# Performance work log

Hardware: AMD Instinct MI355X
Metric: run time of the kernel (lower is better)

The kernel has to match this reference:

```python
import jax, jax.numpy as jnp
import numpy as np

NUM_FEATURES = 50


def _build_port_feature_mask(num_node_features: int = NUM_FEATURES) -> np.ndarray:
    """(F, 6) mask: port p has track if any connect/port-revenue feature for p is nonzero."""
    mask = np.zeros((num_node_features, 6), dtype=np.float32)
    feat_idx = 23
    for i in range(6):
        for j in range(i):
            mask[feat_idx, i] = 1.0
            mask[feat_idx, j] = 1.0
            feat_idx += 1
    for i in range(6):
        for k in range(2):
            mask[38 + i * 2 + k, i] = 1.0
    return mask


def setup_inputs() -> dict:
    key = jax.random.key(0)
    k1, k2 = jax.random.split(key)
    B, N, F = 16, 1024, NUM_FEATURES
    node_features = jax.random.normal(k1, (B, N, F), dtype=jnp.float32)
    direction_matrix = jax.random.randint(k2, (N, N), 0, 7, dtype=jnp.int32)
    port_feature_mask = jnp.asarray(_build_port_feature_mask(F))
    return {
        "node_features": node_features,
        "direction_matrix": direction_matrix,
        "port_feature_mask": port_feature_mask,
    }


def reference(node_features, direction_matrix, port_feature_mask):
    B, N, _ = node_features.shape
    # (B, N, 6): per-hex, per-port track indicator
    port_activity = node_features @ port_feature_mask
    port_has_track = (port_activity > 0).astype(node_features.dtype)

    dir_mat = direction_matrix.astype(jnp.int32)
    adj_mask = (dir_mat != 6).astype(node_features.dtype)  # (N, N)
    dir_clamped = jnp.minimum(dir_mat, 5)                  # (N, N)
    opp_clamped = jnp.minimum((dir_mat + 3) % 6, 5)        # (N, N)

    i_idx = jnp.arange(N)[:, None]  # row index i, broadcasts with (N, N)
    j_idx = jnp.arange(N)[None, :]  # col index j
    # src[b, i, j] = port_has_track[b, i, dir_clamped[i, j]]
    src_ports = port_has_track[:, i_idx, dir_clamped]  # (B, N, N)
    # dst[b, i, j] = port_has_track[b, j, opp_clamped[i, j]]
    dst_ports = port_has_track[:, j_idx, opp_clamped]  # (B, N, N)

    return src_ports * dst_ports * adj_mask[None, :, :]
```

## Files before the change

### kernel.cpp

```cpp
#include <hip/hip_runtime.h>

#define N_NODES 1024
#define B_SZ 16
#define F_SZ 50

typedef float f32x4 __attribute__((ext_vector_type(4)));

__global__ __launch_bounds__(64) void ports_kernel(
        const float* __restrict__ nf,
        unsigned char* __restrict__ bits) {
    int idx = blockIdx.x * 64 + threadIdx.x;
    const float* r = nf + (size_t)idx * F_SZ;

    float f[27];
    #pragma unroll
    for (int q = 0; q < 27; ++q) f[q] = r[23 + q];

    float a0 = (((((f[0]  + f[1])  + f[3])  + f[6])  + f[10]) + f[15]) + f[16];
    float a1 = (((((f[0]  + f[2])  + f[4])  + f[7])  + f[11]) + f[17]) + f[18];
    float a2 = (((((f[1]  + f[2])  + f[5])  + f[8])  + f[12]) + f[19]) + f[20];
    float a3 = (((((f[3]  + f[4])  + f[5])  + f[9])  + f[13]) + f[21]) + f[22];
    float a4 = (((((f[6]  + f[7])  + f[8])  + f[9])  + f[14]) + f[23]) + f[24];
    float a5 = (((((f[10] + f[11]) + f[12]) + f[13]) + f[14]) + f[25]) + f[26];

    unsigned m = 0;
    m |= (a0 > 0.0f) ? 1u  : 0u;
    m |= (a1 > 0.0f) ? 2u  : 0u;
    m |= (a2 > 0.0f) ? 4u  : 0u;
    m |= (a3 > 0.0f) ? 8u  : 0u;
    m |= (a4 > 0.0f) ? 16u : 0u;
    m |= (a5 > 0.0f) ? 32u : 0u;
    bits[idx] = (unsigned char)m;
}

__global__ __launch_bounds__(256) void connect_kernel(
        const int* __restrict__ dir,
        const unsigned char* __restrict__ bits,
        float* __restrict__ out) {
    const int bi = blockIdx.x;
    const int t = threadIdx.x;
    const int b = bi >> 10;
    const int i = bi & (N_NODES - 1);

    int4 d = ((const int4*)(dir + (size_t)i * N_NODES))[t];
    uchar4 dv4 = ((const uchar4*)(bits + b * N_NODES))[t];
    unsigned tb[4] = {dv4.x, dv4.y, dv4.z, dv4.w};
    const unsigned s = bits[b * N_NODES + i];

    int dvv[4] = {d.x, d.y, d.z, d.w};
    f32x4 o;
    #pragma unroll
    for (int k = 0; k < 4; ++k) {
        int dval = dvv[k];
        unsigned am = (dval != 6) ? 1u : 0u;
        unsigned ds = (unsigned)min(dval, 5);
        unsigned os = (unsigned)min((dval + 3) % 6, 5);
        o[k] = ((s >> ds) & (tb[k] >> os) & am & 1u) ? 1.0f : 0.0f;
    }
    __builtin_nontemporal_store(
        o, (f32x4*)(out + (size_t)bi * N_NODES) + t);
}

extern "C" void kernel_launch(void* const* d_in, const int* in_sizes, int n_in,
                              void* d_out, int out_size, void* d_ws, size_t ws_size,
                              hipStream_t stream) {
    const float* nf  = (const float*)d_in[0];
    const int*   dir = (const int*)d_in[1];
    float* out = (float*)d_out;
    unsigned char* bits = (unsigned char*)d_ws;

    ports_kernel<<<(B_SZ * N_NODES) / 64, 64, 0, stream>>>(nf, bits);
    connect_kernel<<<B_SZ * N_NODES, 256, 0, stream>>>(dir, bits, out);
}
```

Baseline: 21.21 us.

## Precompute packed byte direction codes in prep kernel and read bytes in connect

```diff
diff --git a/kernel.cpp b/kernel.cpp
--- a/kernel.cpp
+++ b/kernel.cpp
@@ -6,35 +6,58 @@
 
 typedef float f32x4 __attribute__((ext_vector_type(4)));
 
-__global__ __launch_bounds__(64) void ports_kernel(
+__global__ __launch_bounds__(256) void prep_kernel(
         const float* __restrict__ nf,
-        unsigned char* __restrict__ bits) {
-    int idx = blockIdx.x * 64 + threadIdx.x;
-    const float* r = nf + (size_t)idx * F_SZ;
+        const int* __restrict__ dir,
+        unsigned char* __restrict__ bits,
+        unsigned char* __restrict__ pdir) {
+    const int q = blockIdx.x;
+    const int t = threadIdx.x;
 
-    float f[27];
-    #pragma unroll
-    for (int q = 0; q < 27; ++q) f[q] = r[23 + q];
+    if (q < 64) {
+        const int idx = q * 256 + t;
+        const float* r = nf + (size_t)idx * F_SZ;
+        float f[27];
+        #pragma unroll
+        for (int x = 0; x < 27; ++x) f[x] = r[23 + x];
 
-    float a0 = (((((f[0]  + f[1])  + f[3])  + f[6])  + f[10]) + f[15]) + f[16];
-    float a1 = (((((f[0]  + f[2])  + f[4])  + f[7])  + f[11]) + f[17]) + f[18];
-    float a2 = (((((f[1]  + f[2])  + f[5])  + f[8])  + f[12]) + f[19]) + f[20];
-    float a3 = (((((f[3]  + f[4])  + f[5])  + f[9])  + f[13]) + f[21]) + f[22];
-    float a4 = (((((f[6]  + f[7])  + f[8])  + f[9])  + f[14]) + f[23]) + f[24];
-    float a5 = (((((f[10] + f[11]) + f[12]) + f[13]) + f[14]) + f[25]) + f[26];
+        float a0 = (((((f[0]  + f[1])  + f[3])  + f[6])  + f[10]) + f[15]) + f[16];
+        float a1 = (((((f[0]  + f[2])  + f[4])  + f[7])  + f[11]) + f[17]) + f[18];
+        float a2 = (((((f[1]  + f[2])  + f[5])  + f[8])  + f[12]) + f[19]) + f[20];
+        float a3 = (((((f[3]  + f[4])  + f[5])  + f[9])  + f[13]) + f[21]) + f[22];
+        float a4 = (((((f[6]  + f[7])  + f[8])  + f[9])  + f[14]) + f[23]) + f[24];
+        float a5 = (((((f[10] + f[11]) + f[12]) + f[13]) + f[14]) + f[25]) + f[26];
 
-    unsigned m = 0;
-    m |= (a0 > 0.0f) ? 1u  : 0u;
-    m |= (a1 > 0.0f) ? 2u  : 0u;
-    m |= (a2 > 0.0f) ? 4u  : 0u;
-    m |= (a3 > 0.0f) ? 8u  : 0u;
-    m |= (a4 > 0.0f) ? 16u : 0u;
-    m |= (a5 > 0.0f) ? 32u : 0u;
-    bits[idx] = (unsigned char)m;
+        unsigned m = 0;
+        m |= (a0 > 0.0f) ? 1u  : 0u;
+        m |= (a1 > 0.0f) ? 2u  : 0u;
+        m |= (a2 > 0.0f) ? 4u  : 0u;
+        m |= (a3 > 0.0f) ? 8u  : 0u;
+        m |= (a4 > 0.0f) ? 16u : 0u;
+        m |= (a5 > 0.0f) ? 32u : 0u;
+        bits[idx] = (unsigned char)m;
+    } else {
+        const int e4 = (q - 64) * 256 + t;
+        int4 d = ((const int4*)dir)[e4];
+        int dv[4] = {d.x, d.y, d.z, d.w};
+        unsigned pk[4];
+        #pragma unroll
+        for (int k = 0; k < 4; ++k) {
+            int dval = dv[k];
+            unsigned adj = (dval != 6) ? 1u : 0u;
+            unsigned ds = (unsigned)min(dval, 5);
+            unsigned os = (unsigned)min((dval + 3) % 6, 5);
+            pk[k] = (adj << 6) | (os << 3) | ds;
+        }
+        uchar4 o;
+        o.x = (unsigned char)pk[0]; o.y = (unsigned char)pk[1];
+        o.z = (unsigned char)pk[2]; o.w = (unsigned char)pk[3];
+        ((uchar4*)pdir)[e4] = o;
+    }
 }
 
 __global__ __launch_bounds__(256) void connect_kernel(
-        const int* __restrict__ dir,
+        const unsigned char* __restrict__ pdir,
         const unsigned char* __restrict__ bits,
         float* __restrict__ out) {
     const int bi = blockIdx.x;
@@ -42,23 +65,20 @@
     const int b = bi >> 10;
     const int i = bi & (N_NODES - 1);
 
-    int4 d = ((const int4*)(dir + (size_t)i * N_NODES))[t];
-    uchar4 dv4 = ((const uchar4*)(bits + b * N_NODES))[t];
-    unsigned tb[4] = {dv4.x, dv4.y, dv4.z, dv4.w};
+    uchar4 p4 = ((const uchar4*)(pdir + (size_t)i * N_NODES))[t];
+    uchar4 t4 = ((const uchar4*)(bits + b * N_NODES))[t];
     const unsigned s = bits[b * N_NODES + i];
+    unsigned pv[4] = {p4.x, p4.y, p4.z, p4.w};
+    unsigned tv[4] = {t4.x, t4.y, t4.z, t4.w};
 
-    int dvv[4] = {d.x, d.y, d.z, d.w};
     f32x4 o;
     #pragma unroll
     for (int k = 0; k < 4; ++k) {
-        int dval = dvv[k];
-        unsigned am = (dval != 6) ? 1u : 0u;
-        unsigned ds = (unsigned)min(dval, 5);
-        unsigned os = (unsigned)min((dval + 3) % 6, 5);
-        o[k] = ((s >> ds) & (tb[k] >> os) & am & 1u) ? 1.0f : 0.0f;
+        unsigned p = pv[k];
+        o[k] = ((s >> (p & 7u)) & (tv[k] >> ((p >> 3) & 7u)) & (p >> 6) & 1u)
+                   ? 1.0f : 0.0f;
     }
-    __builtin_nontemporal_store(
-        o, (f32x4*)(out + (size_t)bi * N_NODES) + t);
+    *((f32x4*)(out + (size_t)bi * N_NODES) + t) = o;
 }
 
 extern "C" void kernel_launch(void* const* d_in, const int* in_sizes, int n_in,
@@ -68,7 +88,8 @@
     const int*   dir = (const int*)d_in[1];
     float* out = (float*)d_out;
     unsigned char* bits = (unsigned char*)d_ws;
+    unsigned char* pdir = (unsigned char*)d_ws + 16384;
 
-    ports_kernel<<<(B_SZ * N_NODES) / 64, 64, 0, stream>>>(nf, bits);
-    connect_kernel<<<B_SZ * N_NODES, 256, 0, stream>>>(dir, bits, out);
+    prep_kernel<<<64 + 1024, 256, 0, stream>>>(nf, dir, bits, pdir);
+    connect_kernel<<<B_SZ * N_NODES, 256, 0, stream>>>(pdir, bits, out);
 }
```

Result: no change. 21.23 us (+0.1%).

## Make connect kernel persistent with prefetched next-row loads

Applied to the files above, without the earlier changes.

```diff
diff --git a/kernel.cpp b/kernel.cpp
--- a/kernel.cpp
+++ b/kernel.cpp
@@ -3,6 +3,8 @@
 #define N_NODES 1024
 #define B_SZ 16
 #define F_SZ 50
+#define CBLOCKS 2048
+#define NITER (B_SZ * N_NODES / CBLOCKS)
 
 typedef float f32x4 __attribute__((ext_vector_type(4)));
 
@@ -37,28 +39,40 @@
         const int* __restrict__ dir,
         const unsigned char* __restrict__ bits,
         float* __restrict__ out) {
-    const int bi = blockIdx.x;
+    const int blk = blockIdx.x;
     const int t = threadIdx.x;
-    const int b = bi >> 10;
-    const int i = bi & (N_NODES - 1);
 
-    int4 d = ((const int4*)(dir + (size_t)i * N_NODES))[t];
-    uchar4 dv4 = ((const uchar4*)(bits + b * N_NODES))[t];
-    unsigned tb[4] = {dv4.x, dv4.y, dv4.z, dv4.w};
-    const unsigned s = bits[b * N_NODES + i];
+    int p = blk;
+    int4 d = ((const int4*)(dir + (size_t)(p & (N_NODES - 1)) * N_NODES))[t];
+    uchar4 t4 = ((const uchar4*)(bits + (p >> 10) * N_NODES))[t];
+    unsigned s = bits[(p >> 10) * N_NODES + (p & (N_NODES - 1))];
 
-    int dvv[4] = {d.x, d.y, d.z, d.w};
-    f32x4 o;
     #pragma unroll
-    for (int k = 0; k < 4; ++k) {
-        int dval = dvv[k];
-        unsigned am = (dval != 6) ? 1u : 0u;
-        unsigned ds = (unsigned)min(dval, 5);
-        unsigned os = (unsigned)min((dval + 3) % 6, 5);
-        o[k] = ((s >> ds) & (tb[k] >> os) & am & 1u) ? 1.0f : 0.0f;
+    for (int it = 0; it < NITER; ++it) {
+        const int pc = p;
+        int4 dc = d; uchar4 t4c = t4; unsigned sc = s;
+
+        if (it + 1 < NITER) {
+            p = blk + (it + 1) * CBLOCKS;
+            d  = ((const int4*)(dir + (size_t)(p & (N_NODES - 1)) * N_NODES))[t];
+            t4 = ((const uchar4*)(bits + (p >> 10) * N_NODES))[t];
+            s  = bits[(p >> 10) * N_NODES + (p & (N_NODES - 1))];
+        }
+
+        int dvv[4] = {dc.x, dc.y, dc.z, dc.w};
+        unsigned tv[4] = {t4c.x, t4c.y, t4c.z, t4c.w};
+        f32x4 o;
+        #pragma unroll
+        for (int k = 0; k < 4; ++k) {
+            int dval = dvv[k];
+            unsigned am = (dval != 6) ? 1u : 0u;
+            unsigned ds = (unsigned)min(dval, 5);
+            unsigned os = (unsigned)min((dval + 3) % 6, 5);
+            o[k] = ((sc >> ds) & (tv[k] >> os) & am & 1u) ? 1.0f : 0.0f;
+        }
+        __builtin_nontemporal_store(
+            o, (f32x4*)(out + (size_t)pc * N_NODES) + t);
     }
-    __builtin_nontemporal_store(
-        o, (f32x4*)(out + (size_t)bi * N_NODES) + t);
 }
 
 extern "C" void kernel_launch(void* const* d_in, const int* in_sizes, int n_in,
@@ -70,5 +84,5 @@
     unsigned char* bits = (unsigned char*)d_ws;
 
     ports_kernel<<<(B_SZ * N_NODES) / 64, 64, 0, stream>>>(nf, bits);
-    connect_kernel<<<B_SZ * N_NODES, 256, 0, stream>>>(dir, bits, out);
+    connect_kernel<<<CBLOCKS, 256, 0, stream>>>(dir, bits, out);
 }
```

After: 22.16 us. 1.04x slower.
